# Kernel optimization log

Hardware: AMD Instinct MI355X
Metric: run time of the kernel (lower is better)

Reference implementation:

```python
import jax, jax.numpy as jnp
import numpy as np
from jax import lax

DIM = 180
NH = 6
WS = (16, 16)          # window_size
BWS = (8, 8)           # base_win_size (min of base and window)
HEAD_DIM = DIM // (2 * NH)      # 15
SCALE = HEAD_DIM
POS_DIM = (DIM // 4) // 4       # 11 (DynamicPosBias pos_dim on dim//4)
B, H, W = 2, 256, 256
L = WS[0] * WS[1]               # 256 tokens per window
ML = BWS[0] * BWS[1]            # 64 downsampled tokens
R = L // ML                     # 4, spatial_linear in_features


def _rel_index():
    Hs, Ws = WS
    coords = np.stack(np.meshgrid(np.arange(Hs), np.arange(Ws), indexing='ij')).reshape(2, -1)
    rel = (coords[:, :, None] - coords[:, None, :]).transpose(1, 2, 0)
    rel[..., 0] += Hs - 1
    rel[..., 1] += Ws - 1
    rel[..., 0] *= 2 * Ws - 1
    return jnp.asarray(rel.sum(-1).reshape(-1))  # (L*L,) indices into (2H-1)*(2W-1)


def _bias_grid():
    Hs, Ws = WS
    g = np.stack(np.meshgrid(np.arange(1 - Hs, Hs), np.arange(1 - Ws, Ws), indexing='ij'))
    return jnp.asarray(g.reshape(2, -1).T.astype(np.float32))  # ((2H-1)*(2W-1), 2)

REL_IDX = _rel_index()
BIAS_GRID = _bias_grid()


def _ln(x, g, b):
    m = x.mean(-1, keepdims=True)
    v = ((x - m) ** 2).mean(-1, keepdims=True)
    return (x - m) / jnp.sqrt(v + 1e-5) * g + b


def window_partition(x, ws):
    Bn, Hn, Wn, C = x.shape
    x = x.reshape(Bn, Hn // ws[0], ws[0], Wn // ws[1], ws[1], C)
    return x.transpose(0, 1, 3, 2, 4, 5).reshape(-1, ws[0], ws[1], C)


def window_reverse(w, ws, Hn, Wn):
    Bn = w.shape[0] * (ws[0] * ws[1]) // (Hn * Wn)
    x = w.reshape(Bn, Hn // ws[0], Wn // ws[1], ws[0], ws[1], -1)
    return x.transpose(0, 1, 3, 2, 4, 5).reshape(Bn, Hn, Wn, -1)


def setup_inputs():
    key = jax.random.key(0)
    ks = jax.random.split(key, 16)
    s = 0.02
    rn = lambda k, shape: jax.random.normal(k, shape, jnp.float32) * s
    C5 = DIM // 5
    return {
        'x': jax.random.normal(ks[0], (B, H, W, DIM), jnp.float32),
        'conv1_w': rn(ks[1], (DIM, C5)), 'conv1_b': jnp.zeros((C5,), jnp.float32),
        'conv2_w': rn(ks[2], (3, 3, C5, C5)), 'conv2_b': jnp.zeros((C5,), jnp.float32),
        'conv3_w': rn(ks[3], (C5, DIM)), 'conv3_b': jnp.zeros((DIM,), jnp.float32),
        'dfe_lin_w': rn(ks[4], (DIM, DIM)), 'dfe_lin_b': jnp.zeros((DIM,), jnp.float32),
        'sl_w': rn(ks[5], (R,)), 'sl_b': jnp.zeros((), jnp.float32),
        'pos_proj_w': rn(ks[6], (2, POS_DIM)), 'pos_proj_b': jnp.zeros((POS_DIM,), jnp.float32),
        'ln1_g': jnp.ones((POS_DIM,), jnp.float32), 'ln1_b': jnp.zeros((POS_DIM,), jnp.float32),
        'mlp1_w': rn(ks[7], (POS_DIM, POS_DIM)), 'mlp1_b': jnp.zeros((POS_DIM,), jnp.float32),
        'ln2_g': jnp.ones((POS_DIM,), jnp.float32), 'ln2_b': jnp.zeros((POS_DIM,), jnp.float32),
        'mlp2_w': rn(ks[8], (POS_DIM, POS_DIM)), 'mlp2_b': jnp.zeros((POS_DIM,), jnp.float32),
        'ln3_g': jnp.ones((POS_DIM,), jnp.float32), 'ln3_b': jnp.zeros((POS_DIM,), jnp.float32),
        'mlp3_w': rn(ks[9], (POS_DIM, NH)), 'mlp3_b': jnp.zeros((NH,), jnp.float32),
        'proj_w': rn(ks[10], (DIM, DIM)), 'proj_b': jnp.zeros((DIM,), jnp.float32),
    }


def reference(x, conv1_w, conv1_b, conv2_w, conv2_b, conv3_w, conv3_b,
              dfe_lin_w, dfe_lin_b, sl_w, sl_b, pos_proj_w, pos_proj_b,
              ln1_g, ln1_b, mlp1_w, mlp1_b, ln2_g, ln2_b, mlp2_w, mlp2_b,
              ln3_g, ln3_b, mlp3_w, mlp3_b, proj_w, proj_b):
    xB, xH, xW, xC = x.shape

    # ---- DFE: qv = conv(x) * linear(x), both in NHWC ----
    y = jax.nn.leaky_relu(x @ conv1_w + conv1_b, 0.2)
    y = lax.conv_general_dilated(y, conv2_w, (1, 1), 'SAME',
                                 dimension_numbers=('NHWC', 'HWIO', 'NHWC'))
    y = jax.nn.leaky_relu(y + conv2_b, 0.2)
    y = y @ conv3_w + conv3_b
    qv = y * (x @ dfe_lin_w + dfe_lin_b)            # (B,H,W,C)

    # ---- window partition + q/v head split ----
    qv = window_partition(qv, WS).reshape(-1, L, xC)       # (Bw,L,C)
    Bw = qv.shape[0]
    qv = qv.reshape(Bw, L, 2, NH, HEAD_DIM).transpose(2, 0, 3, 1, 4)
    q, v = qv[0], qv[1]                                    # (Bw,NH,L,hd)

    # ---- spatial self-correlation ----
    mH, mW = BWS
    rH, rW = WS[0] // mH, WS[1] // mW
    v_ = v.reshape(Bw, NH, mH, rH, mW, rW, HEAD_DIM)
    v_ = v_.transpose(0, 1, 2, 4, 6, 3, 5).reshape(Bw, NH, ML, HEAD_DIM, rH * rW)
    vp = jnp.einsum('bhmcr,r->bhmc', v_, sl_w) + sl_b      # (Bw,NH,ML,hd)

    corr = jnp.einsum('bhlc,bhmc->bhlm', q, vp) / SCALE    # (Bw,NH,L,ML)

    # dynamic relative position bias MLP (residual=False)
    p = BIAS_GRID @ pos_proj_w + pos_proj_b
    p = jax.nn.relu(_ln(p, ln1_g, ln1_b)) @ mlp1_w + mlp1_b
    p = jax.nn.relu(_ln(p, ln2_g, ln2_b)) @ mlp2_w + mlp2_b
    p = jax.nn.relu(_ln(p, ln3_g, ln3_b)) @ mlp3_w + mlp3_b  # ((2H-1)*(2W-1), NH)

    rpb = p[REL_IDX].reshape(L, mH, rH, mW, rW, NH)
    rpb = rpb.transpose(0, 1, 3, 5, 2, 4).reshape(L, ML, NH, rH * rW).mean(-1)
    rpb = rpb.transpose(2, 0, 1)                            # (NH,L,ML)
    corr = corr + rpb[None]

    x_sp = jnp.einsum('bhlm,bhmc->bhlc', corr, vp)
    x_sp = x_sp.transpose(0, 2, 1, 3).reshape(Bw, L, NH * HEAD_DIM)

    # ---- channel self-correlation ----
    qc = q.transpose(0, 2, 1, 3).reshape(Bw, L, NH * HEAD_DIM)
    vc = v.transpose(0, 2, 1, 3).reshape(Bw, L, NH * HEAD_DIM)
    cc = jnp.einsum('blc,bld->bcd', qc, vc) / L
    x_ch = jnp.einsum('bcd,bld->blc', cc, vc)

    # ---- merge windows, concat, project ----
    half = xC // 2
    x_sp = window_reverse(x_sp.reshape(-1, WS[0], WS[1], half), WS, xH, xW)
    x_ch = window_reverse(x_ch.reshape(-1, WS[0], WS[1], half), WS, xH, xW)
    out = jnp.concatenate([x_sp, x_ch], -1) @ proj_w + proj_b
    return out
```

## Files before the change

### kernel.cpp

```cpp
#include <hip/hip_runtime.h>
#include <hip/hip_fp16.h>

typedef unsigned int uint32;
typedef _Float16 f16;
typedef f16 f16x4 __attribute__((ext_vector_type(4)));
typedef f16 f16x8 __attribute__((ext_vector_type(8)));
typedef float f32x4 __attribute__((ext_vector_type(4)));

union U8 { f16x8 v; uint4 u4; uint2 u2[2]; f16 h[8]; };

__device__ __forceinline__ float h2f(__half v) { return __half2float(v); }
__device__ __forceinline__ __half f2h(float v) { return __float2half(v); }

__global__ __launch_bounds__(256) void k1_conv1(const float* __restrict__ X,
                                                const float* __restrict__ W1,
                                                const float* __restrict__ B1,
                                                __half* __restrict__ T1) {
  __shared__ float sm[60 * 132 + 60 * 36];
  float* Xt = sm;
  float* Ws = sm + 60 * 132;
  int t = threadIdx.x;
  int p0 = blockIdx.x * 128;
  bool act = t < 144;
  int r0 = (t / 9) * 4, c0 = (t % 9) * 4;
  float acc[2][16];
#pragma unroll
  for (int h = 0; h < 2; ++h)
#pragma unroll
    for (int i = 0; i < 16; ++i) acc[h][i] = 0.f;

  for (int chunk = 0; chunk < 3; ++chunk) {
    __syncthreads();
    int kc = chunk * 60;
    for (int i = t; i < 128 * 60; i += 256) {
      int m = i / 60, k = i % 60;
      Xt[k * 132 + m] = X[(size_t)(p0 + m) * 180 + kc + k];
    }
    for (int i = t; i < 60 * 36; i += 256) {
      int k = i / 36, c = i % 36;
      Ws[k * 36 + c] = W1[(kc + k) * 36 + c];
    }
    __syncthreads();
    if (act) {
      for (int k = 0; k < 60; ++k) {
        float4 a0 = *(const float4*)&Xt[k * 132 + r0];
        float4 a1 = *(const float4*)&Xt[k * 132 + r0 + 64];
        float4 b  = *(const float4*)&Ws[k * 36 + c0];
        float av0[4] = {a0.x, a0.y, a0.z, a0.w};
        float av1[4] = {a1.x, a1.y, a1.z, a1.w};
        float bv[4]  = {b.x, b.y, b.z, b.w};
#pragma unroll
        for (int i = 0; i < 4; ++i)
#pragma unroll
          for (int j = 0; j < 4; ++j) {
            acc[0][i * 4 + j] += av0[i] * bv[j];
            acc[1][i * 4 + j] += av1[i] * bv[j];
          }
      }
    }
  }
  if (!act) return;
  float bb[4];
#pragma unroll
  for (int i = 0; i < 4; ++i) bb[i] = B1[c0 + i];
#pragma unroll
  for (int h = 0; h < 2; ++h)
#pragma unroll
    for (int ri = 0; ri < 4; ++ri) {
      int p = p0 + h * 64 + r0 + ri;
      __half* o = T1 + (size_t)p * 36 + c0;
      __half2 h01, h23;
      float v0 = acc[h][ri * 4 + 0] + bb[0];
      float v1 = acc[h][ri * 4 + 1] + bb[1];
      float v2 = acc[h][ri * 4 + 2] + bb[2];
      float v3 = acc[h][ri * 4 + 3] + bb[3];
      h01.x = f2h(v0 > 0.f ? v0 : 0.2f * v0);
      h01.y = f2h(v1 > 0.f ? v1 : 0.2f * v1);
      h23.x = f2h(v2 > 0.f ? v2 : 0.2f * v2);
      h23.y = f2h(v3 > 0.f ? v3 : 0.2f * v3);
      *(__half2*)o = h01;
      *(__half2*)(o + 2) = h23;
    }
}

__global__ __launch_bounds__(256) void k0_w2(const float* __restrict__ W2,
                                             f16* __restrict__ W2T) {
  int i = blockIdx.x * 256 + threadIdx.x;
  if (i < 17280) {
    int tap = i / 1920, rem = i % 1920, n = rem / 40, k = rem % 40;
    W2T[i] = (n < 36 && k < 36) ? (f16)W2[(tap * 36 + k) * 36 + n] : (f16)0;
  }
}

__global__ __launch_bounds__(256) void k2_conv2(const __half* __restrict__ T1,
                                                const f16* __restrict__ W2T,
                                                const float* __restrict__ B2,
                                                __half* __restrict__ T2) {
  __shared__ __align__(16) f16 ins[3 * 132 * 40];
  int t = threadIdx.x;
  int p0 = blockIdx.x * 128;
  int b = p0 >> 16, y = (p0 >> 8) & 255, x0 = p0 & 255;

  const uint32* T1u = (const uint32*)T1;
  uint32* insu = (uint32*)ins;
  for (int i = t; i < 7920; i += 256) {
    int kh = i / 2640, rem = i % 2640;
    int xx = rem / 20, u = rem % 20;
    int ry = y + kh - 1, gx = x0 + xx - 1;
    uint32 v = 0u;
    if (u < 18 && xx < 130 && (unsigned)ry < 256u && (unsigned)gx < 256u)
      v = T1u[((size_t)((b * 256 + ry) * 256 + gx)) * 18 + u];
    insu[i] = v;
  }
  __syncthreads();

  int lane = t & 63, wave = t >> 6;
  int lm = lane & 15, lq = lane >> 4;
  const f16x8 zero8 = {(f16)0,(f16)0,(f16)0,(f16)0,(f16)0,(f16)0,(f16)0,(f16)0};

  f32x4 acc[2][3];
#pragma unroll
  for (int mt = 0; mt < 2; ++mt)
#pragma unroll
    for (int nt = 0; nt < 3; ++nt) acc[mt][nt] = (f32x4){0.f, 0.f, 0.f, 0.f};

#pragma unroll
  for (int kh = 0; kh < 3; ++kh) {
#pragma unroll
    for (int kw = 0; kw < 3; ++kw) {
      int tap = kh * 3 + kw;
      f16x8 a0[2], a1[2];
#pragma unroll
      for (int mt = 0; mt < 2; ++mt) {
        int xx = wave * 32 + mt * 16 + lm + kw;
        const f16* ar = &ins[(kh * 132 + xx) * 40];
        a0[mt] = *(const f16x8*)&ar[lq * 8];
        a1[mt] = (lq == 0) ? *(const f16x8*)&ar[32] : zero8;
      }
#pragma unroll
      for (int nt = 0; nt < 3; ++nt) {
        const f16* br = &W2T[(tap * 48 + nt * 16 + lm) * 40];
        f16x8 b0 = *(const f16x8*)&br[lq * 8];
        f16x8 b1 = (lq == 0) ? *(const f16x8*)&br[32] : zero8;
#pragma unroll
        for (int mt = 0; mt < 2; ++mt) {
          acc[mt][nt] = __builtin_amdgcn_mfma_f32_16x16x32_f16(
              a0[mt], b0, acc[mt][nt], 0, 0, 0);
          acc[mt][nt] = __builtin_amdgcn_mfma_f32_16x16x32_f16(
              a1[mt], b1, acc[mt][nt], 0, 0, 0);
        }
      }
    }
  }

  float bb[3];
#pragma unroll
  for (int nt = 0; nt < 3; ++nt) {
    int co = nt * 16 + lm;
    bb[nt] = (co < 36) ? B2[co] : 0.f;
  }
#pragma unroll
  for (int mt = 0; mt < 2; ++mt) {
#pragma unroll
    for (int reg = 0; reg < 4; ++reg) {
      int p = p0 + wave * 32 + mt * 16 + lq * 4 + reg;
      __half* o = T2 + (size_t)p * 36;
#pragma unroll
      for (int nt = 0; nt < 3; ++nt) {
        int co = nt * 16 + lm;
        if (co < 36) {
          float v = acc[mt][nt][reg] + bb[nt];
          o[co] = f2h(v > 0.f ? v : 0.2f * v);
        }
      }
    }
  }
}

__global__ __launch_bounds__(256) void k0_wt(const float* __restrict__ SW3,
                                             const float* __restrict__ SWD,
                                             f16* __restrict__ WT3,
                                             f16* __restrict__ WTD) {
  int tid = blockIdx.x * 256 + threadIdx.x;
  int stride = gridDim.x * 256;
  for (int i = tid; i < 192 * 40; i += stride) {
    int n = i / 40, k = i % 40;
    WT3[i] = (n < 180 && k < 36) ? (f16)SW3[k * 180 + n] : (f16)0;
  }
  for (int i = tid; i < 192 * 192; i += stride) {
    int n = i / 192, k = i % 192;
    WTD[i] = (n < 180 && k < 180) ? (f16)SWD[k * 180 + n] : (f16)0;
  }
}

__global__ __launch_bounds__(256) void k0_pw(const float* __restrict__ SPW,
                                             f16* __restrict__ PWT) {
  int tid = blockIdx.x * 256 + threadIdx.x;
  int stride = gridDim.x * 256;
  for (int i = tid; i < 192 * 192; i += stride) {
    int n = i / 192, k = i % 192;
    PWT[i] = (n < 180 && k < 180) ? (f16)SPW[k * 180 + n] : (f16)0;
  }
}

__global__ __launch_bounds__(256) void k3_qv(const float* __restrict__ X,
                                             const __half* __restrict__ T2,
                                             const f16* __restrict__ WT3,
                                             const f16* __restrict__ WTD,
                                             const float* __restrict__ B3,
                                             const float* __restrict__ BD,
                                             __half* __restrict__ QX) {
  int t = threadIdx.x;
  int p0 = blockIdx.x * 128;
  int lane = t & 63, wave = t >> 6;
  int lm = lane & 15, lq = lane >> 4;

  const f16x8 zero8 = {(f16)0,(f16)0,(f16)0,(f16)0,(f16)0,(f16)0,(f16)0,(f16)0};

  f16x8 ax[6][2];
  f16x8 at0[2];
  f16x8 at1[2];
#pragma unroll
  for (int mt = 0; mt < 2; ++mt) {
    int row = p0 + wave * 32 + mt * 16 + lm;
    const float* xr = X + (size_t)row * 180;
#pragma unroll
    for (int ch = 0; ch < 6; ++ch) {
      int k0 = ch * 32 + lq * 8;
      U8 v; v.u4 = (uint4){0u, 0u, 0u, 0u};
      if (k0 + 8 <= 180) {
        float4 a = *(const float4*)&xr[k0];
        float4 b = *(const float4*)&xr[k0 + 4];
        v.h[0]=(f16)a.x; v.h[1]=(f16)a.y; v.h[2]=(f16)a.z; v.h[3]=(f16)a.w;
        v.h[4]=(f16)b.x; v.h[5]=(f16)b.y; v.h[6]=(f16)b.z; v.h[7]=(f16)b.w;
      } else if (k0 < 180) {
        float4 a = *(const float4*)&xr[k0];
        v.h[0]=(f16)a.x; v.h[1]=(f16)a.y; v.h[2]=(f16)a.z; v.h[3]=(f16)a.w;
      }
      ax[ch][mt] = v.v;
    }
    const f16* tr = (const f16*)T2 + (size_t)row * 36;
    U8 tv;
    tv.u2[0] = *(const uint2*)&tr[lq * 8];
    tv.u2[1] = *(const uint2*)&tr[lq * 8 + 4];
    at0[mt] = tv.v;
    U8 t1v; t1v.u4 = (uint4){0u, 0u, 0u, 0u};
    if (lq == 0) t1v.u2[0] = *(const uint2*)&tr[32];
    at1[mt] = t1v.v;
  }

  for (int bn = 0; bn < 4; ++bn) {
    int n0 = bn * 48;
    f32x4 accC[2][3], accD[2][3];
#pragma unroll
    for (int i = 0; i < 2; ++i)
#pragma unroll
      for (int j = 0; j < 3; ++j) {
        accC[i][j] = (f32x4){0.f, 0.f, 0.f, 0.f};
        accD[i][j] = (f32x4){0.f, 0.f, 0.f, 0.f};
      }

#pragma unroll
    for (int nt = 0; nt < 3; ++nt) {
      int n = n0 + nt * 16 + lm;
      f16x8 b0 = *(const f16x8*)&WT3[n * 40 + lq * 8];
      f16x8 b1 = (lq == 0) ? *(const f16x8*)&WT3[n * 40 + 32] : zero8;
#pragma unroll
      for (int mt = 0; mt < 2; ++mt) {
        accC[mt][nt] = __builtin_amdgcn_mfma_f32_16x16x32_f16(
            at0[mt], b0, accC[mt][nt], 0, 0, 0);
        accC[mt][nt] = __builtin_amdgcn_mfma_f32_16x16x32_f16(
            at1[mt], b1, accC[mt][nt], 0, 0, 0);
      }
    }

#pragma unroll
    for (int ch = 0; ch < 6; ++ch) {
#pragma unroll
      for (int nt = 0; nt < 3; ++nt) {
        int n = n0 + nt * 16 + lm;
        f16x8 bf = *(const f16x8*)&WTD[n * 192 + ch * 32 + lq * 8];
        accD[0][nt] = __builtin_amdgcn_mfma_f32_16x16x32_f16(
            ax[ch][0], bf, accD[0][nt], 0, 0, 0);
        accD[1][nt] = __builtin_amdgcn_mfma_f32_16x16x32_f16(
            ax[ch][1], bf, accD[1][nt], 0, 0, 0);
      }
    }

    float cb[3], db[3];
#pragma unroll
    for (int nt = 0; nt < 3; ++nt) {
      int col = n0 + nt * 16 + lm;
      cb[nt] = (col < 180) ? B3[col] : 0.f;
      db[nt] = (col < 180) ? BD[col] : 0.f;
    }
#pragma unroll
    for (int mt = 0; mt < 2; ++mt) {
#pragma unroll
      for (int reg = 0; reg < 4; ++reg) {
        int p = p0 + wave * 32 + mt * 16 + lq * 4 + reg;
        int b = p >> 16, y = (p >> 8) & 255, x = p & 255;
        int wi = (b << 8) | ((y >> 4) << 4) | (x >> 4);
        int l = ((y & 15) << 4) | (x & 15);
        __half* orow = QX + ((size_t)(wi * 256 + l)) * 180;
#pragma unroll
        for (int nt = 0; nt < 3; ++nt) {
          int col = n0 + nt * 16 + lm;
          if (col < 180)
            orow[col] = f2h((accC[mt][nt][reg] + cb[nt]) *
                            (accD[mt][nt][reg] + db[nt]) * 64.f);
        }
      }
    }
  }
}

__device__ __forceinline__ void ln_relu11(const float* p, const float* g,
                                          const float* b, float* r) {
  float m = 0.f;
#pragma unroll
  for (int j = 0; j < 11; ++j) m += p[j];
  m *= (1.0f / 11.0f);
  float v = 0.f;
#pragma unroll
  for (int j = 0; j < 11; ++j) { float d = p[j] - m; v += d * d; }
  v *= (1.0f / 11.0f);
  float inv = 1.0f / sqrtf(v + 1e-5f);
#pragma unroll
  for (int j = 0; j < 11; ++j) {
    float xn = (p[j] - m) * inv * g[j] + b[j];
    r[j] = fmaxf(xn, 0.f);
  }
}
__device__ __forceinline__ void mm11(const float* r, const float* W,
                                     const float* b, float* o) {
#pragma unroll
  for (int j2 = 0; j2 < 11; ++j2) {
    float s = b[j2];
#pragma unroll
    for (int j = 0; j < 11; ++j) s += r[j] * W[j * 11 + j2];
    o[j2] = s;
  }
}

__global__ __launch_bounds__(256) void k5a_posmlp(
    const float* PPW, const float* PPB,
    const float* LN1G, const float* LN1B, const float* M1W, const float* M1B,
    const float* LN2G, const float* LN2B, const float* M2W, const float* M2B,
    const float* LN3G, const float* LN3B, const float* M3W, const float* M3B,
    float* __restrict__ PTAB) {
  int t = blockIdx.x * 256 + threadIdx.x;
  if (t >= 961) return;
  float g0 = (float)(t / 31) - 15.0f;
  float g1 = (float)(t % 31) - 15.0f;
  float p[11], r[11];
#pragma unroll
  for (int j = 0; j < 11; ++j)
    p[j] = g0 * PPW[j] + g1 * PPW[11 + j] + PPB[j];
  ln_relu11(p, LN1G, LN1B, r);
  mm11(r, M1W, M1B, p);
  ln_relu11(p, LN2G, LN2B, r);
  mm11(r, M2W, M2B, p);
  ln_relu11(p, LN3G, LN3B, r);
#pragma unroll
  for (int h = 0; h < 6; ++h) {
    float s = M3B[h];
#pragma unroll
    for (int j = 0; j < 11; ++j) s += r[j] * M3W[j * 6 + h];
    PTAB[t * 6 + h] = s;
  }
}

__global__ __launch_bounds__(256) void k5b_rpb(const float* __restrict__ PTAB,
                                               float* __restrict__ RPB) {
  int t = blockIdx.x * 256 + threadIdx.x;
  int m = t & 63;
  int l = (t >> 6) & 255;
  int h = t >> 14;
  int mh = m >> 3, mw = m & 7;
  int qr = l >> 4, qc = l & 15;
  float s = 0.f;
#pragma unroll
  for (int rh = 0; rh < 2; ++rh)
#pragma unroll
    for (int rw = 0; rw < 2; ++rw) {
      int dr = qr - (mh * 2 + rh) + 15;
      int dc = qc - (mw * 2 + rw) + 15;
      s += PTAB[(dr * 31 + dc) * 6 + h];
    }
  RPB[t] = 0.25f * s;
}

__global__ __launch_bounds__(256) void k7a_cc(const __half* __restrict__ QX,
                                              float* __restrict__ CC) {
  __shared__ __half qs[64 * 90];
  __shared__ __half vs[64 * 90];
  int wi = blockIdx.x, t = threadIdx.x;
  int c0 = (t % 15) * 6, d0 = (t / 15) * 6;
  bool act = t < 225;
  float acc[36];
#pragma unroll
  for (int i = 0; i < 36; ++i) acc[i] = 0.f;
  const uint32* G = (const uint32*)(QX + (size_t)wi * 46080);
  uint32* qsw = (uint32*)qs;
  uint32* vsw = (uint32*)vs;
  for (int pass = 0; pass < 4; ++pass) {
    __syncthreads();
    for (int i = t; i < 2880; i += 256) {
      int l = i / 45, k = i % 45;
      int gw = (pass * 64 + l) * 90;
      qsw[l * 45 + k] = G[gw + k];
      vsw[l * 45 + k] = G[gw + 45 + k];
    }
    __syncthreads();
    if (act) {
      for (int l = 0; l < 64; ++l) {
        const __half2* qh = (const __half2*)&qs[l * 90 + c0];
        const __half2* vh = (const __half2*)&vs[l * 90 + d0];
        float a[6], b[6];
#pragma unroll
        for (int k = 0; k < 3; ++k) {
          __half2 x = qh[k];
          a[2 * k] = __low2float(x); a[2 * k + 1] = __high2float(x);
          __half2 y = vh[k];
          b[2 * k] = __low2float(y); b[2 * k + 1] = __high2float(y);
        }
#pragma unroll
        for (int i = 0; i < 6; ++i)
#pragma unroll
          for (int j = 0; j < 6; ++j) acc[i * 6 + j] += a[i] * b[j];
      }
    }
  }
  if (act) {
    const float s = 1.0f / (256.0f * 4096.0f);
#pragma unroll
    for (int i = 0; i < 6; ++i)
#pragma unroll
      for (int j = 0; j < 6; ++j)
        CC[((size_t)(wi * 90 + c0 + i)) * 90 + d0 + j] = acc[i * 6 + j] * s;
  }
}

__global__ __launch_bounds__(256) void kA_xsp(__half* __restrict__ QX,
                                              const float* __restrict__ RPB,
                                              const float* __restrict__ SLW,
                                              const float* __restrict__ SLB) {
  __shared__ __align__(16) unsigned char SM[80384];
  f16* U   = (f16*)SM;
  f16* vpS = (f16*)(SM + 53248);
  f16* vpT = (f16*)(SM + 66560);
  int wi = blockIdx.x, t = threadIdx.x;
  __half* QW = QX + (size_t)wi * 46080;
  const uint32* G = (const uint32*)QW;
  uint32* Uw = (uint32*)U;

  for (int i = t; i < 11520; i += 256) {
    int l = i / 45, k = i % 45;
    Uw[l * 45 + k] = G[l * 90 + 45 + k];
  }
  __syncthreads();
  float w0 = SLW[0], w1 = SLW[1], w2 = SLW[2], w3 = SLW[3];
  float sb = SLB[0];
  for (int e = t; e < 6144; e += 256) {
    int m = e & 63, idx = e >> 6;
    int c = idx & 15, h = idx >> 4;
    f16 val = (f16)0;
    if (c < 15) {
      int ch = h * 15 + c;
      int lb = (m >> 3) * 32 + (m & 7) * 2;
      float s = w0 * (float)U[lb * 90 + ch] + w1 * (float)U[(lb + 1) * 90 + ch]
              + w2 * (float)U[(lb + 16) * 90 + ch] + w3 * (float)U[(lb + 17) * 90 + ch];
      val = (f16)(s * 4.f + sb * 256.f);
    }
    vpS[m * 104 + idx] = val;
    vpT[idx * 72 + m] = val;
  }
  __syncthreads();
  for (int j = t; j < 1536; j += 256) {
    int h = j >> 8, l = j & 255;
    U[l * 104 + h * 16 + 15] = (f16)0;
  }
  for (int i = t; i < 11520; i += 256) {
    int l = i / 45, k = i % 45;
    union { uint32 w; f16 h[2]; } cv;
    cv.w = G[l * 90 + k];
    int cg0 = 2 * k, cg1 = 2 * k + 1;
    int h0 = cg0 / 15, c0 = cg0 - h0 * 15;
    int h1 = cg1 / 15, c1 = cg1 - h1 * 15;
    U[l * 104 + h0 * 16 + c0] = cv.h[0];
    U[l * 104 + h1 * 16 + c1] = cv.h[1];
  }
  __syncthreads();

  int lane = t & 63, w = t >> 6;
  int lm = lane & 15, lq = lane >> 4;
  const float invA = 1.0f / 960.0f;
  for (int h = 0; h < 6; ++h) {
    f16x4 a1[4], b1[4];
#pragma unroll
    for (int mt = 0; mt < 4; ++mt)
      a1[mt] = *(const f16x4*)&vpS[(mt * 16 + lm) * 104 + h * 16 + lq * 4];
#pragma unroll
    for (int lt = 0; lt < 4; ++lt)
      b1[lt] = *(const f16x4*)&U[(w * 64 + lt * 16 + lm) * 104 + h * 16 + lq * 4];
    f32x4 acc1[4][4];
#pragma unroll
    for (int mt = 0; mt < 4; ++mt)
#pragma unroll
      for (int lt = 0; lt < 4; ++lt)
        acc1[mt][lt] = __builtin_amdgcn_mfma_f32_16x16x16f16(
            a1[mt], b1[lt], (f32x4){0.f, 0.f, 0.f, 0.f}, 0, 0, 0);
    f16x4 b2[4][4];
#pragma unroll
    for (int lt = 0; lt < 4; ++lt) {
      int l = w * 64 + lt * 16 + lm;
      const float* rp = RPB + ((size_t)(h * 256 + l)) * 64;
#pragma unroll
      for (int mt = 0; mt < 4; ++mt) {
        float4 rv = *(const float4*)&rp[mt * 16 + lq * 4];
        f16x4 bb;
        bb[0] = (f16)(acc1[mt][lt][0] * invA + rv.x * 256.f);
        bb[1] = (f16)(acc1[mt][lt][1] * invA + rv.y * 256.f);
        bb[2] = (f16)(acc1[mt][lt][2] * invA + rv.z * 256.f);
        bb[3] = (f16)(acc1[mt][lt][3] * invA + rv.w * 256.f);
        b2[mt][lt] = bb;
      }
    }
    f16x4 a2[4];
#pragma unroll
    for (int kt = 0; kt < 4; ++kt)
      a2[kt] = *(const f16x4*)&vpT[(h * 16 + lm) * 72 + kt * 16 + lq * 4];
#pragma unroll
    for (int lt = 0; lt < 4; ++lt) {
      f32x4 acc2 = (f32x4){0.f, 0.f, 0.f, 0.f};
#pragma unroll
      for (int kt = 0; kt < 4; ++kt)
        acc2 = __builtin_amdgcn_mfma_f32_16x16x16f16(a2[kt], b2[kt][lt], acc2, 0, 0, 0);
      int l = w * 64 + lt * 16 + lm;
      __half* orow = QW + l * 180 + h * 15;
#pragma unroll
      for (int reg = 0; reg < 4; ++reg) {
        int c = lq * 4 + reg;
        if (c < 15) orow[c] = f2h(acc2[reg] * 0.125f);
      }
    }
  }
}

__global__ __launch_bounds__(256) void kB_xch(__half* __restrict__ QX,
                                              const float* __restrict__ CC) {
  __shared__ __align__(16) f16 vA[256 * 104];
  __shared__ __align__(16) f16 ccB[96 * 104];
  int wi = blockIdx.x, t = threadIdx.x;
  __half* QW = QX + (size_t)wi * 46080;
  const uint32* G = (const uint32*)QW;
  uint32* vAw = (uint32*)vA;
  for (int i = t; i < 12288; i += 256) {
    int l = i / 48, kk = i % 48;
    vAw[l * 52 + kk] = (kk < 45) ? G[l * 90 + 45 + kk] : 0u;
  }
  const float* ccg = CC + (size_t)wi * 8100;
  uint32* ccw = (uint32*)ccB;
  for (int i = t; i < 4992; i += 256) {
    int c = i / 52, dd = i % 52;
    uint32 out = 0u;
    if (c < 90 && dd < 45) {
      float2 f = *(const float2*)&ccg[c * 90 + dd * 2];
      union { uint32 w; f16 h[2]; } cv;
      cv.h[0] = (f16)(f.x * 65536.f);
      cv.h[1] = (f16)(f.y * 65536.f);
      out = cv.w;
    }
    ccw[c * 52 + dd] = out;
  }
  __syncthreads();
  int lane = t & 63, w = t >> 6;
  int lm = lane & 15, lq = lane >> 4;
  f32x4 acc[4][6];
#pragma unroll
  for (int mt = 0; mt < 4; ++mt)
#pragma unroll
    for (int nt = 0; nt < 6; ++nt) acc[mt][nt] = (f32x4){0.f, 0.f, 0.f, 0.f};
  for (int kc = 0; kc < 3; ++kc) {
    f16x8 af[4], bf[6];
#pragma unroll
    for (int mt = 0; mt < 4; ++mt)
      af[mt] = *(const f16x8*)&vA[(w * 64 + mt * 16 + lm) * 104 + kc * 32 + lq * 8];
#pragma unroll
    for (int nt = 0; nt < 6; ++nt)
      bf[nt] = *(const f16x8*)&ccB[(nt * 16 + lm) * 104 + kc * 32 + lq * 8];
#pragma unroll
    for (int mt = 0; mt < 4; ++mt)
#pragma unroll
      for (int nt = 0; nt < 6; ++nt)
        acc[mt][nt] = __builtin_amdgcn_mfma_f32_16x16x32_f16(
            af[mt], bf[nt], acc[mt][nt], 0, 0, 0);
  }
#pragma unroll
  for (int mt = 0; mt < 4; ++mt) {
#pragma unroll
    for (int reg = 0; reg < 4; ++reg) {
      int l = w * 64 + mt * 16 + lq * 4 + reg;
      __half* orow = QW + l * 180 + 90;
#pragma unroll
      for (int nt = 0; nt < 6; ++nt) {
        int c = nt * 16 + lm;
        if (c < 90) orow[c] = f2h(acc[mt][nt][reg] * 0.001953125f);
      }
    }
  }
}

__global__ __launch_bounds__(256) void k8_proj(const __half* __restrict__ XS,
                                               const f16* __restrict__ PWT,
                                               const float* __restrict__ PB,
                                               float* __restrict__ OUT) {
  int t = threadIdx.x;
  int w0r = blockIdx.x * 128;
  int lane = t & 63, wave = t >> 6;
  int lm = lane & 15, lq = lane >> 4;

  f16x8 ax[6][2];
#pragma unroll
  for (int mt = 0; mt < 2; ++mt) {
    int row = w0r + wave * 32 + mt * 16 + lm;
    const f16* xr = (const f16*)XS + (size_t)row * 180;
#pragma unroll
    for (int ch = 0; ch < 6; ++ch) {
      int k0 = ch * 32 + lq * 8;
      U8 v; v.u4 = (uint4){0u, 0u, 0u, 0u};
      if (k0 + 8 <= 180) {
        v.u2[0] = *(const uint2*)&xr[k0];
        v.u2[1] = *(const uint2*)&xr[k0 + 4];
      } else if (k0 < 180) {
        v.u2[0] = *(const uint2*)&xr[k0];
      }
      ax[ch][mt] = v.v;
    }
  }

  for (int bn = 0; bn < 4; ++bn) {
    int n0 = bn * 48;
    f32x4 acc[2][3];
#pragma unroll
    for (int i = 0; i < 2; ++i)
#pragma unroll
      for (int j = 0; j < 3; ++j) acc[i][j] = (f32x4){0.f, 0.f, 0.f, 0.f};

#pragma unroll
    for (int ch = 0; ch < 6; ++ch) {
#pragma unroll
      for (int nt = 0; nt < 3; ++nt) {
        int n = n0 + nt * 16 + lm;
        f16x8 bf = *(const f16x8*)&PWT[n * 192 + ch * 32 + lq * 8];
        acc[0][nt] = __builtin_amdgcn_mfma_f32_16x16x32_f16(
            ax[ch][0], bf, acc[0][nt], 0, 0, 0);
        acc[1][nt] = __builtin_amdgcn_mfma_f32_16x16x32_f16(
            ax[ch][1], bf, acc[1][nt], 0, 0, 0);
      }
    }

    float pb[3];
#pragma unroll
    for (int nt = 0; nt < 3; ++nt) {
      int col = n0 + nt * 16 + lm;
      pb[nt] = (col < 180) ? PB[col] : 0.f;
    }
    const float inv = 1.0f / 8192.0f;
#pragma unroll
    for (int mt = 0; mt < 2; ++mt) {
#pragma unroll
      for (int reg = 0; reg < 4; ++reg) {
        int w = w0r + wave * 32 + mt * 16 + lq * 4 + reg;
        int wi = w >> 8, l = w & 255;
        int b = wi >> 8, wy = (wi >> 4) & 15, wx = wi & 15;
        int ly = l >> 4, lx = l & 15;
        int p = (b << 16) | (((wy << 4) | ly) << 8) | ((wx << 4) | lx);
        float* orow = OUT + (size_t)p * 180;
#pragma unroll
        for (int nt = 0; nt < 3; ++nt) {
          int col = n0 + nt * 16 + lm;
          if (col < 180) orow[col] = acc[mt][nt][reg] * inv + pb[nt];
        }
      }
    }
  }
}

extern "C" void kernel_launch(void* const* d_in, const int* in_sizes, int n_in,
                              void* d_out, int out_size, void* d_ws, size_t ws_size,
                              hipStream_t stream) {
  const float* X    = (const float*)d_in[0];
  const float* W1   = (const float*)d_in[1];
  const float* B1   = (const float*)d_in[2];
  const float* W2   = (const float*)d_in[3];
  const float* B2   = (const float*)d_in[4];
  const float* W3   = (const float*)d_in[5];
  const float* B3c  = (const float*)d_in[6];
  const float* WD   = (const float*)d_in[7];
  const float* BD   = (const float*)d_in[8];
  const float* SLW  = (const float*)d_in[9];
  const float* SLB  = (const float*)d_in[10];
  const float* PPW  = (const float*)d_in[11];
  const float* PPB  = (const float*)d_in[12];
  const float* LN1G = (const float*)d_in[13];
  const float* LN1B = (const float*)d_in[14];
  const float* M1W  = (const float*)d_in[15];
  const float* M1B  = (const float*)d_in[16];
  const float* LN2G = (const float*)d_in[17];
  const float* LN2B = (const float*)d_in[18];
  const float* M2W  = (const float*)d_in[19];
  const float* M2B  = (const float*)d_in[20];
  const float* LN3G = (const float*)d_in[21];
  const float* LN3B = (const float*)d_in[22];
  const float* M3W  = (const float*)d_in[23];
  const float* M3B  = (const float*)d_in[24];
  const float* PW   = (const float*)d_in[25];
  const float* PB   = (const float*)d_in[26];
  float* OUT = (float*)d_out;

  char* ws = (char*)d_ws;
  f16*   W2T  = (f16*)(ws);
  __half* QX  = (__half*)(ws);
  __half* T1  = (__half*)(ws + 47185920);
  __half* T2  = (__half*)(ws + 56623104);
  float* PTAB = (float*)(ws + 47185920);
  float* RPB  = (float*)(ws + 47212544);
  f16*   WT3  = (f16*)(ws + 47605760);
  f16*   WTD  = (f16*)(ws + 47621120);
  float* CC   = (float*)(ws + 47605760);
  f16*   PWT  = (f16*)(ws + 64194560);

  hipLaunchKernelGGL(k0_w2, dim3(68), dim3(256), 0, stream, W2, W2T);
  hipLaunchKernelGGL(k1_conv1, dim3(1024), dim3(256), 0, stream, X, W1, B1, T1);
  hipLaunchKernelGGL(k2_conv2, dim3(1024), dim3(256), 0, stream, T1, W2T, B2, T2);
  hipLaunchKernelGGL(k0_wt, dim3(144), dim3(256), 0, stream, W3, WD, WT3, WTD);
  hipLaunchKernelGGL(k3_qv, dim3(1024), dim3(256), 0, stream, X, T2, WT3, WTD, B3c, BD, QX);
  hipLaunchKernelGGL(k0_pw, dim3(144), dim3(256), 0, stream, PW, PWT);
  hipLaunchKernelGGL(k5a_posmlp, dim3(4), dim3(256), 0, stream,
                     PPW, PPB, LN1G, LN1B, M1W, M1B, LN2G, LN2B, M2W, M2B,
                     LN3G, LN3B, M3W, M3B, PTAB);
  hipLaunchKernelGGL(k5b_rpb, dim3(384), dim3(256), 0, stream, PTAB, RPB);
  hipLaunchKernelGGL(k7a_cc, dim3(512), dim3(256), 0, stream, QX, CC);
  hipLaunchKernelGGL(kA_xsp, dim3(512), dim3(256), 0, stream, QX, RPB, SLW, SLB);
  hipLaunchKernelGGL(kB_xch, dim3(512), dim3(256), 0, stream, QX, CC);
  hipLaunchKernelGGL(k8_proj, dim3(1024), dim3(256), 0, stream, QX, PWT, PB, OUT);
}
```

Baseline: 542.0 us.

## Rewrite conv1 1x1 projection using fp16 MFMA with pre-transposed padded weights

The first 1x1 convolution (180->36 channels) moves from an fp32 scalar FMA kernel with an LDS-transposed input to an MFMA 16x16x32 fp16 kernel. Each wave loads its rows of X straight from global memory, converts them to fp16 in registers, and multiplies against a weight matrix that a new prep kernel transposes and pads to 48x192. This removes the LDS staging and the scalar inner loop. It costs fp16 input rounding, wasted padded work in the third N tile, and one extra small launch. Output stores become scattered per-element half writes.

```diff
diff --git a/kernel.cpp b/kernel.cpp
--- a/kernel.cpp
+++ b/kernel.cpp
@@ -12,75 +12,87 @@
 __device__ __forceinline__ float h2f(__half v) { return __half2float(v); }
 __device__ __forceinline__ __half f2h(float v) { return __float2half(v); }
 
+__global__ __launch_bounds__(256) void k0_w1(const float* __restrict__ W1,
+                                             f16* __restrict__ W1T) {
+  int i = blockIdx.x * 256 + threadIdx.x;
+  if (i < 9216) {
+    int n = i / 192, k = i % 192;
+    W1T[i] = (n < 36 && k < 180) ? (f16)W1[k * 36 + n] : (f16)0;
+  }
+}
+
 __global__ __launch_bounds__(256) void k1_conv1(const float* __restrict__ X,
-                                                const float* __restrict__ W1,
+                                                const f16* __restrict__ W1T,
                                                 const float* __restrict__ B1,
                                                 __half* __restrict__ T1) {
-  __shared__ float sm[60 * 132 + 60 * 36];
-  float* Xt = sm;
-  float* Ws = sm + 60 * 132;
   int t = threadIdx.x;
   int p0 = blockIdx.x * 128;
-  bool act = t < 144;
-  int r0 = (t / 9) * 4, c0 = (t % 9) * 4;
-  float acc[2][16];
-#pragma unroll
-  for (int h = 0; h < 2; ++h)
-#pragma unroll
-    for (int i = 0; i < 16; ++i) acc[h][i] = 0.f;
-
-  for (int chunk = 0; chunk < 3; ++chunk) {
-    __syncthreads();
-    int kc = chunk * 60;
-    for (int i = t; i < 128 * 60; i += 256) {
-      int m = i / 60, k = i % 60;
-      Xt[k * 132 + m] = X[(size_t)(p0 + m) * 180 + kc + k];
-    }
-    for (int i = t; i < 60 * 36; i += 256) {
-      int k = i / 36, c = i % 36;
-      Ws[k * 36 + c] = W1[(kc + k) * 36 + c];
-    }
-    __syncthreads();
-    if (act) {
-      for (int k = 0; k < 60; ++k) {
-        float4 a0 = *(const float4*)&Xt[k * 132 + r0];
-        float4 a1 = *(const float4*)&Xt[k * 132 + r0 + 64];
-        float4 b  = *(const float4*)&Ws[k * 36 + c0];
-        float av0[4] = {a0.x, a0.y, a0.z, a0.w};
-        float av1[4] = {a1.x, a1.y, a1.z, a1.w};
-        float bv[4]  = {b.x, b.y, b.z, b.w};
-#pragma unroll
-        for (int i = 0; i < 4; ++i)
-#pragma unroll
-          for (int j = 0; j < 4; ++j) {
-            acc[0][i * 4 + j] += av0[i] * bv[j];
-            acc[1][i * 4 + j] += av1[i] * bv[j];
-          }
-      }
-    }
-  }
-  if (!act) return;
-  float bb[4];
-#pragma unroll
-  for (int i = 0; i < 4; ++i) bb[i] = B1[c0 + i];
-#pragma unroll
-  for (int h = 0; h < 2; ++h)
-#pragma unroll
-    for (int ri = 0; ri < 4; ++ri) {
-      int p = p0 + h * 64 + r0 + ri;
-      __half* o = T1 + (size_t)p * 36 + c0;
-      __half2 h01, h23;
-      float v0 = acc[h][ri * 4 + 0] + bb[0];
-      float v1 = acc[h][ri * 4 + 1] + bb[1];
-      float v2 = acc[h][ri * 4 + 2] + bb[2];
-      float v3 = acc[h][ri * 4 + 3] + bb[3];
-      h01.x = f2h(v0 > 0.f ? v0 : 0.2f * v0);
-      h01.y = f2h(v1 > 0.f ? v1 : 0.2f * v1);
-      h23.x = f2h(v2 > 0.f ? v2 : 0.2f * v2);
-      h23.y = f2h(v3 > 0.f ? v3 : 0.2f * v3);
-      *(__half2*)o = h01;
-      *(__half2*)(o + 2) = h23;
-    }
+  int lane = t & 63, wave = t >> 6;
+  int lm = lane & 15, lq = lane >> 4;
+
+  f16x8 ax[6][2];
+#pragma unroll
+  for (int mt = 0; mt < 2; ++mt) {
+    int row = p0 + wave * 32 + mt * 16 + lm;
+    const float* xr = X + (size_t)row * 180;
+#pragma unroll
+    for (int ch = 0; ch < 6; ++ch) {
+      int k0 = ch * 32 + lq * 8;
+      U8 v; v.u4 = (uint4){0u, 0u, 0u, 0u};
+      if (k0 + 8 <= 180) {
+        float4 a = *(const float4*)&xr[k0];
+        float4 b = *(const float4*)&xr[k0 + 4];
+        v.h[0]=(f16)a.x; v.h[1]=(f16)a.y; v.h[2]=(f16)a.z; v.h[3]=(f16)a.w;
+        v.h[4]=(f16)b.x; v.h[5]=(f16)b.y; v.h[6]=(f16)b.z; v.h[7]=(f16)b.w;
+      } else if (k0 < 180) {
+        float4 a = *(const float4*)&xr[k0];
+        v.h[0]=(f16)a.x; v.h[1]=(f16)a.y; v.h[2]=(f16)a.z; v.h[3]=(f16)a.w;
+      }
+      ax[ch][mt] = v.v;
+    }
+  }
+
+  f32x4 acc[2][3];
+#pragma unroll
+  for (int mt = 0; mt < 2; ++mt)
+#pragma unroll
+    for (int nt = 0; nt < 3; ++nt) acc[mt][nt] = (f32x4){0.f, 0.f, 0.f, 0.f};
+
+#pragma unroll
+  for (int ch = 0; ch < 6; ++ch) {
+#pragma unroll
+    for (int nt = 0; nt < 3; ++nt) {
+      int n = nt * 16 + lm;
+      f16x8 bf = *(const f16x8*)&W1T[n * 192 + ch * 32 + lq * 8];
+      acc[0][nt] = __builtin_amdgcn_mfma_f32_16x16x32_f16(
+          ax[ch][0], bf, acc[0][nt], 0, 0, 0);
+      acc[1][nt] = __builtin_amdgcn_mfma_f32_16x16x32_f16(
+          ax[ch][1], bf, acc[1][nt], 0, 0, 0);
+    }
+  }
+
+  float bb[3];
+#pragma unroll
+  for (int nt = 0; nt < 3; ++nt) {
+    int co = nt * 16 + lm;
+    bb[nt] = (co < 36) ? B1[co] : 0.f;
+  }
+#pragma unroll
+  for (int mt = 0; mt < 2; ++mt) {
+#pragma unroll
+    for (int reg = 0; reg < 4; ++reg) {
+      int p = p0 + wave * 32 + mt * 16 + lq * 4 + reg;
+      __half* o = T1 + (size_t)p * 36;
+#pragma unroll
+      for (int nt = 0; nt < 3; ++nt) {
+        int co = nt * 16 + lm;
+        if (co < 36) {
+          float v = acc[mt][nt][reg] + bb[nt];
+          o[co] = f2h(v > 0.f ? v : 0.2f * v);
+        }
+      }
+    }
+  }
 }
 
 __global__ __launch_bounds__(256) void k0_w2(const float* __restrict__ W2,
@@ -722,6 +734,7 @@
 
   char* ws = (char*)d_ws;
   f16*   W2T  = (f16*)(ws);
+  f16*   W1T  = (f16*)(ws + 34560);
   __half* QX  = (__half*)(ws);
   __half* T1  = (__half*)(ws + 47185920);
   __half* T2  = (__half*)(ws + 56623104);
@@ -733,7 +746,8 @@
   f16*   PWT  = (f16*)(ws + 64194560);
 
   hipLaunchKernelGGL(k0_w2, dim3(68), dim3(256), 0, stream, W2, W2T);
-  hipLaunchKernelGGL(k1_conv1, dim3(1024), dim3(256), 0, stream, X, W1, B1, T1);
+  hipLaunchKernelGGL(k0_w1, dim3(36), dim3(256), 0, stream, W1, W1T);
+  hipLaunchKernelGGL(k1_conv1, dim3(1024), dim3(256), 0, stream, X, W1T, B1, T1);
   hipLaunchKernelGGL(k2_conv2, dim3(1024), dim3(256), 0, stream, T1, W2T, B2, T2);
   hipLaunchKernelGGL(k0_wt, dim3(144), dim3(256), 0, stream, W3, WD, WT3, WTD);
   hipLaunchKernelGGL(k3_qv, dim3(1024), dim3(256), 0, stream, X, T2, WT3, WTD, B3c, BD, QX);
```

New measurement: 522.2 us. 3.7% less time.
